# Performance work log

Measured on AMD Instinct MI355X. Metric: run time of the kernel, lower is better.

The kernel has to match this reference:

```python
import jax, jax.numpy as jnp
import numpy as np

ROI = 7
NMS_THR = 0.01
NMS_SIZE = 100


def crop_and_resize(fmap, boxes, crop):
    # fmap [H,W,C], boxes [N,4] normalized (y1,x1,y2,x2) -> [N,crop,crop,C]
    H, W, C = fmap.shape
    t = jnp.linspace(0.0, 1.0, crop)
    ys = (boxes[:, 0:1] + (boxes[:, 2:3] - boxes[:, 0:1]) * t) * (H - 1)  # [N,crop]
    xs = (boxes[:, 1:2] + (boxes[:, 3:4] - boxes[:, 1:2]) * t) * (W - 1)
    y0 = jnp.clip(jnp.floor(ys), 0, H - 1).astype(jnp.int32)
    x0 = jnp.clip(jnp.floor(xs), 0, W - 1).astype(jnp.int32)
    y1 = jnp.clip(y0 + 1, 0, H - 1)
    x1 = jnp.clip(x0 + 1, 0, W - 1)
    wy = (ys - y0)[:, :, None, None]
    wx = (xs - x0)[:, None, :, None]
    Y0, Y1 = y0[:, :, None], y1[:, :, None]
    X0, X1 = x0[:, None, :], x1[:, None, :]
    f00 = fmap[Y0, X0]; f01 = fmap[Y0, X1]
    f10 = fmap[Y1, X0]; f11 = fmap[Y1, X1]
    return (f00 * (1 - wy) * (1 - wx) + f01 * (1 - wy) * wx
            + f10 * wy * (1 - wx) + f11 * wy * wx)


def iou_matrix(b):
    # b [N,4] (x1,y1,x2,y2)
    area = jnp.maximum(b[:, 2] - b[:, 0], 0) * jnp.maximum(b[:, 3] - b[:, 1], 0)
    lt = jnp.maximum(b[:, None, :2], b[None, :, :2])
    rb = jnp.minimum(b[:, None, 2:], b[None, :, 2:])
    wh = jnp.maximum(rb - lt, 0.0)
    inter = wh[..., 0] * wh[..., 1]
    return inter / (area[:, None] + area[None, :] - inter + 1e-8)


def nms(boxes, scores, thr, max_out):
    # greedy NMS, fixed-size output (pads with lowest-ranked boxes when fewer survive)
    N = boxes.shape[0]
    order = jnp.argsort(-scores)
    M = iou_matrix(boxes[order])
    idx = jnp.arange(N)
    def body(i, keep):
        sup = (M[i] > thr) & (idx > i) & keep[i]
        return keep & ~sup
    keep = jax.lax.fori_loop(0, N, body, jnp.ones(N, dtype=bool))
    rank = jnp.where(keep, idx, N + idx)
    sel = jnp.argsort(rank)[:max_out]
    return order[sel]


def make_boxes(key, n):
    kc, ks = jax.random.split(key)
    c = jax.random.uniform(kc, (n, 2), minval=0.1, maxval=0.9)
    s = jax.random.uniform(ks, (n, 2), minval=0.02, maxval=0.15)
    lo = jnp.clip(c - s / 2, 0.0, 1.0)
    hi = jnp.clip(c + s / 2, 0.0, 1.0)
    return jnp.concatenate([lo, hi], axis=1)  # (y1,x1,y2,x2)


def setup_inputs() -> dict:
    key = jax.random.key(0)
    ks = jax.random.split(key, 12)
    N, D, Hd = 1024, ROI * ROI * 32, 2048
    img_boxes = make_boxes(ks[0], N)
    bev_boxes = make_boxes(ks[1], N)
    bev_boxes_abs = bev_boxes[:, jnp.array([1, 0, 3, 2])] * 80.0  # (x1,y1,x2,y2) in meters
    def w(k, shape, fan_in):
        return jax.random.normal(k, shape, jnp.float32) * (2.0 / fan_in) ** 0.5
    return {
        'img_feat_map': jax.random.uniform(ks[2], (1, 360, 1200, 32), jnp.float32),
        'bev_feat_map': jax.random.uniform(ks[3], (1, 700, 800, 32), jnp.float32),
        'img_boxes': img_boxes,
        'bev_boxes': bev_boxes,
        'bev_boxes_abs': bev_boxes_abs,
        'img_mask': jnp.ones((1, 1, 1, 1), jnp.float32),
        'bev_mask': jnp.ones((1, 1, 1, 1), jnp.float32),
        'W1': w(ks[4], (D, Hd), D), 'b1': jnp.zeros((Hd,), jnp.float32),
        'W2': w(ks[5], (Hd, Hd), Hd), 'b2': jnp.zeros((Hd,), jnp.float32),
        'Wc': w(ks[6], (Hd, 2), Hd), 'bc': jnp.zeros((2,), jnp.float32),
        'Wo': w(ks[7], (Hd, 10), Hd), 'bo': jnp.zeros((10,), jnp.float32),
        'Wa': w(ks[8], (Hd, 2), Hd), 'ba': jnp.zeros((2,), jnp.float32),
    }


def reference(img_feat_map, bev_feat_map, img_boxes, bev_boxes, bev_boxes_abs,
              img_mask, bev_mask, W1, b1, W2, b2, Wc, bc, Wo, bo, Wa, ba):
    # ROI align on masked feature maps
    rois_rgb = crop_and_resize((img_mask * img_feat_map)[0], img_boxes, ROI)
    rois_bev = crop_and_resize((bev_mask * bev_feat_map)[0], bev_boxes, ROI)
    # mean fusion
    fused = (rois_rgb + rois_bev) / (img_mask + bev_mask)  # [N,7,7,32]
    # predictor
    x = fused.reshape(fused.shape[0], -1)
    h = jax.nn.relu(x @ W1 + b1)
    h = jax.nn.relu(h @ W2 + b2)
    obj = h @ Wc + bc            # [N,2]
    off = h @ Wo + bo            # [N,10]
    ang = h @ Wa + ba            # [N,2]
    obj_soft = jax.nn.softmax(obj, axis=1)
    orient = jnp.arctan2(ang[:, 1], ang[:, 0])  # convert_angle_to_orientation
    # offset-adjusted BEV boxes for NMS
    pb = bev_boxes_abs + 0.1 * off[:, :4]
    boxes = jnp.stack([jnp.minimum(pb[:, 0], pb[:, 2]), jnp.minimum(pb[:, 1], pb[:, 3]),
                       jnp.maximum(pb[:, 0], pb[:, 2]), jnp.maximum(pb[:, 1], pb[:, 3])], axis=1)
    scores = jnp.max(obj[:, 1:], axis=1)
    ti = nms(jax.lax.stop_gradient(boxes), jax.lax.stop_gradient(scores), NMS_THR, NMS_SIZE)
    # [100, 2 + 4 + 1]: softmax scores, pred bev boxes, orientations
    return jnp.concatenate([obj_soft[ti], boxes[ti], orient[ti][:, None]], axis=1)
```

## Files before the change

kernel.cpp:

```cpp
#include <hip/hip_runtime.h>
#include <math.h>

#define NBOX 1024
#define ROI_N 7
#define CH 32
#define FEAT (ROI_N*ROI_N*CH)
#define K1PAD 1664
#define HD 2048
#define NMS_THR_F 0.01f
#define NMS_OUT 100
#define MTRI_WORDS 8704

typedef _Float16 f16;
typedef f16 f16x4 __attribute__((ext_vector_type(4)));
typedef f16 f16x8 __attribute__((ext_vector_type(8)));
typedef float f32x4 __attribute__((ext_vector_type(4)));

__device__ __forceinline__ void split_f16(float v, f16& h, f16& l) {
  h = (f16)v;
  l = (f16)((v - (float)h) * 4096.0f);
}

__device__ __forceinline__ void gload_lds16(const void* g, void* l) {
  __builtin_amdgcn_global_load_lds(
      (const __attribute__((address_space(1))) unsigned int*)g,
      (__attribute__((address_space(3))) unsigned int*)l, 16, 0, 0);
}

#define B_ROI 1024
#define B_C1  (64*26)
#define B_C2  (64*32)
#define B_INIT 2048
#define B_HT  112

__device__ void roi_part(int b, int tid,
    const float* __restrict__ img, const float* __restrict__ bev,
    const float* __restrict__ img_boxes, const float* __restrict__ bev_boxes,
    float mi, float mb, f16* __restrict__ xh, f16* __restrict__ xl)
{
  const float denom = mi + mb;
  if (tid >= 196) {
    const int g = tid - 196;
    if (g < 12) {
      f16x8 z = {};
      *(f16x8*)&xh[(size_t)b*K1PAD + FEAT + g*8] = z;
      *(f16x8*)&xl[(size_t)b*K1PAD + FEAT + g*8] = z;
    }
    return;
  }
  const int cell = tid >> 2, cg = (tid & 3) * 8;
  const int ti = cell / ROI_N, tj = cell - ti*ROI_N;
  const float tt_i = (ti == 6) ? 1.0f : ti * (1.0f/6.0f);
  const float tt_j = (tj == 6) ? 1.0f : tj * (1.0f/6.0f);

  float vi[8], vb[8];
  {
    const int H = 360, W = 1200;
    const float iy0 = img_boxes[b*4+0], ix0 = img_boxes[b*4+1];
    const float iy1 = img_boxes[b*4+2], ix1 = img_boxes[b*4+3];
    const float ys = (iy0 + (iy1 - iy0) * tt_i) * (float)(H-1);
    const float xs = (ix0 + (ix1 - ix0) * tt_j) * (float)(W-1);
    int y0 = (int)floorf(ys); y0 = y0 < 0 ? 0 : (y0 > H-1 ? H-1 : y0);
    int x0 = (int)floorf(xs); x0 = x0 < 0 ? 0 : (x0 > W-1 ? W-1 : x0);
    const int y1 = (y0+1 > H-1) ? H-1 : y0+1;
    const int x1 = (x0+1 > W-1) ? W-1 : x0+1;
    const float wy = ys - (float)y0, wx = xs - (float)x0;
    const float w00 = (1.0f-wy)*(1.0f-wx), w01 = (1.0f-wy)*wx;
    const float w10 = wy*(1.0f-wx),        w11 = wy*wx;
    const float* p00 = &img[(y0*W + x0)*CH + cg];
    const float* p01 = &img[(y0*W + x1)*CH + cg];
    const float* p10 = &img[(y1*W + x0)*CH + cg];
    const float* p11 = &img[(y1*W + x1)*CH + cg];
#pragma unroll
    for (int q = 0; q < 2; ++q) {
      const float4 f00 = *(const float4*)(p00 + q*4);
      const float4 f01 = *(const float4*)(p01 + q*4);
      const float4 f10 = *(const float4*)(p10 + q*4);
      const float4 f11 = *(const float4*)(p11 + q*4);
      vi[q*4+0] = f00.x*w00 + f01.x*w01 + f10.x*w10 + f11.x*w11;
      vi[q*4+1] = f00.y*w00 + f01.y*w01 + f10.y*w10 + f11.y*w11;
      vi[q*4+2] = f00.z*w00 + f01.z*w01 + f10.z*w10 + f11.z*w11;
      vi[q*4+3] = f00.w*w00 + f01.w*w01 + f10.w*w10 + f11.w*w11;
    }
  }
  {
    const int H = 700, W = 800;
    const float by0 = bev_boxes[b*4+0], bx0 = bev_boxes[b*4+1];
    const float by1 = bev_boxes[b*4+2], bx1 = bev_boxes[b*4+3];
    const float ys = (by0 + (by1 - by0) * tt_i) * (float)(H-1);
    const float xs = (bx0 + (bx1 - bx0) * tt_j) * (float)(W-1);
    int y0 = (int)floorf(ys); y0 = y0 < 0 ? 0 : (y0 > H-1 ? H-1 : y0);
    int x0 = (int)floorf(xs); x0 = x0 < 0 ? 0 : (x0 > W-1 ? W-1 : x0);
    const int y1 = (y0+1 > H-1) ? H-1 : y0+1;
    const int x1 = (x0+1 > W-1) ? W-1 : x0+1;
    const float wy = ys - (float)y0, wx = xs - (float)x0;
    const float w00 = (1.0f-wy)*(1.0f-wx), w01 = (1.0f-wy)*wx;
    const float w10 = wy*(1.0f-wx),        w11 = wy*wx;
    const float* p00 = &bev[(y0*W + x0)*CH + cg];
    const float* p01 = &bev[(y0*W + x1)*CH + cg];
    const float* p10 = &bev[(y1*W + x0)*CH + cg];
    const float* p11 = &bev[(y1*W + x1)*CH + cg];
#pragma unroll
    for (int q = 0; q < 2; ++q) {
      const float4 f00 = *(const float4*)(p00 + q*4);
      const float4 f01 = *(const float4*)(p01 + q*4);
      const float4 f10 = *(const float4*)(p10 + q*4);
      const float4 f11 = *(const float4*)(p11 + q*4);
      vb[q*4+0] = f00.x*w00 + f01.x*w01 + f10.x*w10 + f11.x*w11;
      vb[q*4+1] = f00.y*w00 + f01.y*w01 + f10.y*w10 + f11.y*w11;
      vb[q*4+2] = f00.z*w00 + f01.z*w01 + f10.z*w10 + f11.z*w11;
      vb[q*4+3] = f00.w*w00 + f01.w*w01 + f10.w*w10 + f11.w*w11;
    }
  }
  f16x8 h8, l8;
#pragma unroll
  for (int q = 0; q < 8; ++q) {
    f16 h, l;
    split_f16((mi*vi[q] + mb*vb[q]) / denom, h, l);
    h8[q] = h; l8[q] = l;
  }
  const size_t o = (size_t)b*K1PAD + cell*32 + cg;
  *(f16x8*)&xh[o] = h8;
  *(f16x8*)&xl[o] = l8;
}

__global__ __launch_bounds__(256) void prep_kernel(
    const float* __restrict__ img, const float* __restrict__ bev,
    const float* __restrict__ img_boxes, const float* __restrict__ bev_boxes,
    const float* __restrict__ img_mask, const float* __restrict__ bev_mask,
    f16* __restrict__ xh, f16* __restrict__ xl,
    const float* __restrict__ W1, f16* __restrict__ Wt1h, f16* __restrict__ Wt1l,
    const float* __restrict__ W2, f16* __restrict__ Wt2h, f16* __restrict__ Wt2l,
    const float* __restrict__ b1, const float* __restrict__ b2,
    float4* __restrict__ h1f, float4* __restrict__ h2f,
    const float* __restrict__ Wc, const float* __restrict__ Wo,
    const float* __restrict__ Wa, float* __restrict__ Wcat)
{
  __shared__ float t[64][33];
  const int g = blockIdx.x;
  const int tid = threadIdx.x;

  if (g < B_ROI) {
    roi_part(g, tid, img, bev, img_boxes, bev_boxes, img_mask[0], bev_mask[0], xh, xl);
    return;
  }
  if (g >= B_ROI + B_C1 + B_C2 + B_INIT) {
    const int idx = (g - (B_ROI + B_C1 + B_C2 + B_INIT))*256 + tid;
    const int j = idx >> 11, k = idx & (HD-1);
    float v;
    if (j < 2)       v = Wc[k*2 + j];
    else if (j < 12) v = Wo[k*10 + (j-2)];
    else             v = Wa[k*2 + (j-12)];
    Wcat[idx] = v;
    return;
  }
  const float* W; f16 *Wh, *Wl; int K, Kpad, cb;
  if (g < B_ROI + B_C1) { cb = g - B_ROI;        W = W1; Wh = Wt1h; Wl = Wt1l; K = FEAT; Kpad = K1PAD; }
  else if (g < B_ROI + B_C1 + B_C2) { cb = g - B_ROI - B_C1; W = W2; Wh = Wt2h; Wl = Wt2l; K = HD; Kpad = HD; }
  else {
    const int ib = g - B_ROI - B_C1 - B_C2;
    const int idx = ib*256 + tid;
    const int c4 = idx & (HD/4 - 1);
    h1f[idx] = *(const float4*)&b1[c4*4];
    h2f[idx] = *(const float4*)&b2[c4*4];
    return;
  }
  const int nt = cb & 63, kt = cb >> 6;
  const int n0 = nt * 32, k0 = kt * 64;
#pragma unroll
  for (int p = 0; p < 8; ++p) {
    const int idx = tid + p*256;
    const int kk = idx >> 5, nn = idx & 31;
    const int k = k0 + kk;
    t[kk][nn] = (k < K) ? W[(size_t)k*HD + n0 + nn] : 0.0f;
  }
  __syncthreads();
  const int nn = tid >> 3;
  const int kg = (tid & 7) * 8;
  f16x8 h8, l8;
#pragma unroll
  for (int q = 0; q < 8; ++q) {
    f16 h, l;
    split_f16(t[kg + q][nn], h, l);
    h8[q] = h; l8[q] = l;
  }
  *(f16x8*)&Wh[(size_t)(n0+nn)*Kpad + k0 + kg] = h8;
  *(f16x8*)&Wl[(size_t)(n0+nn)*Kpad + k0 + kg] = l8;
}

__global__ __launch_bounds__(256) void split_relu_kernel(
    const float* __restrict__ in, f16* __restrict__ oh, f16* __restrict__ ol)
{
  const int idx = blockIdx.x*256 + threadIdx.x;
  const float4 v = *(const float4*)&in[idx*4];
  f16x4 h4, l4;
  { f16 h,l; split_f16(fmaxf(v.x,0.0f),h,l); h4[0]=h; l4[0]=l; }
  { f16 h,l; split_f16(fmaxf(v.y,0.0f),h,l); h4[1]=h; l4[1]=l; }
  { f16 h,l; split_f16(fmaxf(v.z,0.0f),h,l); h4[2]=h; l4[2]=l; }
  { f16 h,l; split_f16(fmaxf(v.w,0.0f),h,l); h4[3]=h; l4[3]=l; }
  *(f16x4*)&oh[idx*4] = h4;
  *(f16x4*)&ol[idx*4] = l4;
}

#define STAGE(BUF, KK)                                                        \
  do {                                                                        \
    _Pragma("unroll")                                                         \
    for (int q_ = 0; q_ < 8; ++q_) {                                          \
      const int r_ = q_*16 + lr;                                              \
      const int sg_ = lg ^ ((r_ >> 1) & 3);                                   \
      gload_lds16(&sarr[(size_t)(rbase + r_)*K + (KK) + sg_*8],               \
                  lbase + (BUF)*16384 + q_*512);                              \
    }                                                                         \
  } while (0)

__global__ __launch_bounds__(256, 2) void gemm_sk(
    const f16* __restrict__ Ah_g, const f16* __restrict__ Al_g,
    const f16* __restrict__ Bh_g, const f16* __restrict__ Bl_g,
    float* __restrict__ Cout, int M, int N, int K, int kchunk)
{
  __shared__ __align__(16) f16 lds[2][4][128*32];
  const int tid = threadIdx.x;

  const int g = blockIdx.x;
  const int xcd = g & 7, c = g >> 3;
  const int nb = xcd*2 + (c & 1);
  const int mb = (c >> 1) & 7;
  const int zb = c >> 4;
  const int m0 = mb * 128, n0 = nb * 128;
  const int kb = zb * kchunk, ke = kb + kchunk;

  const int wid = tid >> 6, lane = tid & 63;
  const int wr = wid >> 1, wc = wid & 1;
  const int frow = lane & 15, fkg = lane >> 4;
  const int swz = (fkg ^ ((frow >> 1) & 3)) * 8;

  const f16* sarr; int rbase;
  if (wid == 0)      { sarr = Ah_g; rbase = m0; }
  else if (wid == 1) { sarr = Al_g; rbase = m0; }
  else if (wid == 2) { sarr = Bh_g; rbase = n0; }
  else               { sarr = Bl_g; rbase = n0; }
  f16* lbase = &lds[0][wid][0];
  const int lr = lane >> 2, lg = lane & 3;

  f32x4 acc1[4][4], acc2[4][4];
#pragma unroll
  for (int i = 0; i < 4; ++i)
#pragma unroll
    for (int j = 0; j < 4; ++j)
#pragma unroll
      for (int r = 0; r < 4; ++r) { acc1[i][j][r] = 0.0f; acc2[i][j][r] = 0.0f; }

  STAGE(0, kb);
  __syncthreads();
  int cur = 0;
  for (int kk = kb; kk < ke; kk += 32) {
    if (kk + 32 < ke) STAGE(cur ^ 1, kk + 32);

    const f16* bc_ = &lds[cur][0][0];
    f16x8 bh[4], bl[4];
#pragma unroll
    for (int j = 0; j < 4; ++j) {
      const int rr = wc*64 + j*16 + frow;
      bh[j] = *(const f16x8*)(bc_ + 8192  + rr*32 + swz);
      bl[j] = *(const f16x8*)(bc_ + 12288 + rr*32 + swz);
    }
#pragma unroll
    for (int i = 0; i < 4; ++i) {
      const int rr = wr*64 + i*16 + frow;
      const f16x8 ah = *(const f16x8*)(bc_ +        rr*32 + swz);
      const f16x8 al = *(const f16x8*)(bc_ + 4096 + rr*32 + swz);
#pragma unroll
      for (int j = 0; j < 4; ++j) {
        acc1[i][j] = __builtin_amdgcn_mfma_f32_16x16x32_f16(ah, bh[j], acc1[i][j], 0, 0, 0);
        acc2[i][j] = __builtin_amdgcn_mfma_f32_16x16x32_f16(ah, bl[j], acc2[i][j], 0, 0, 0);
        acc2[i][j] = __builtin_amdgcn_mfma_f32_16x16x32_f16(al, bh[j], acc2[i][j], 0, 0, 0);
      }
    }
    __syncthreads();
    cur ^= 1;
  }

  const float s = 1.0f / 4096.0f;
#pragma unroll
  for (int i = 0; i < 4; ++i)
#pragma unroll
    for (int j = 0; j < 4; ++j) {
      const int col = n0 + wc*64 + j*16 + frow;
#pragma unroll
      for (int r = 0; r < 4; ++r) {
        const int row = m0 + wr*64 + i*16 + fkg*4 + r;
        atomicAdd(&Cout[(size_t)row*N + col], acc1[i][j][r] + acc2[i][j][r] * s);
      }
    }
}

__global__ __launch_bounds__(256) void heads_kernel(
    const float* __restrict__ h2f, const float* __restrict__ Wcat,
    const float* __restrict__ bc, const float* __restrict__ bo,
    const float* __restrict__ ba, const float* __restrict__ bev_abs,
    float* __restrict__ obj_soft, float* __restrict__ boxes,
    float* __restrict__ orient, float* __restrict__ scores)
{
  const int r = blockIdx.x;
  const int tid = threadIdx.x;
  const int k0 = tid * 8;
  float4 hv0 = *(const float4*)&h2f[(size_t)r*HD + k0];
  float4 hv1 = *(const float4*)&h2f[(size_t)r*HD + k0 + 4];
  hv0.x = fmaxf(hv0.x, 0.0f); hv0.y = fmaxf(hv0.y, 0.0f);
  hv0.z = fmaxf(hv0.z, 0.0f); hv0.w = fmaxf(hv0.w, 0.0f);
  hv1.x = fmaxf(hv1.x, 0.0f); hv1.y = fmaxf(hv1.y, 0.0f);
  hv1.z = fmaxf(hv1.z, 0.0f); hv1.w = fmaxf(hv1.w, 0.0f);

  float acc[14];
#pragma unroll
  for (int j = 0; j < 14; ++j) {
    const float4 w0 = *(const float4*)&Wcat[j*HD + k0];
    const float4 w1 = *(const float4*)&Wcat[j*HD + k0 + 4];
    acc[j] = hv0.x*w0.x + hv0.y*w0.y + hv0.z*w0.z + hv0.w*w0.w
           + hv1.x*w1.x + hv1.y*w1.y + hv1.z*w1.z + hv1.w*w1.w;
  }
  __shared__ float red[14][256];
#pragma unroll
  for (int j = 0; j < 14; ++j) red[j][tid] = acc[j];
  __syncthreads();
  for (int s = 128; s > 0; s >>= 1) {
    if (tid < s) {
#pragma unroll
      for (int j = 0; j < 14; ++j) red[j][tid] += red[j][tid + s];
    }
    __syncthreads();
  }
  if (tid == 0) {
    const float obj0 = red[0][0] + bc[0];
    const float obj1 = red[1][0] + bc[1];
    const float off0 = red[2][0] + bo[0];
    const float off1 = red[3][0] + bo[1];
    const float off2 = red[4][0] + bo[2];
    const float off3 = red[5][0] + bo[3];
    const float a0 = red[12][0] + ba[0];
    const float a1 = red[13][0] + ba[1];

    const float m  = fmaxf(obj0, obj1);
    const float e0 = expf(obj0 - m), e1 = expf(obj1 - m);
    const float se = e0 + e1;
    obj_soft[r*2+0] = e0 / se;
    obj_soft[r*2+1] = e1 / se;
    orient[r] = atan2f(a1, a0);

    const float pb0 = bev_abs[r*4+0] + 0.1f*off0;
    const float pb1 = bev_abs[r*4+1] + 0.1f*off1;
    const float pb2 = bev_abs[r*4+2] + 0.1f*off2;
    const float pb3 = bev_abs[r*4+3] + 0.1f*off3;
    boxes[r*4+0] = fminf(pb0, pb2);
    boxes[r*4+1] = fminf(pb1, pb3);
    boxes[r*4+2] = fmaxf(pb0, pb2);
    boxes[r*4+3] = fmaxf(pb1, pb3);
    scores[r] = obj1;
  }
}

__global__ __launch_bounds__(128) void sort_kernel(
    const float* __restrict__ scores, const float* __restrict__ boxes,
    int* __restrict__ order, float4* __restrict__ sboxes, float* __restrict__ sarea)
{
  __shared__ float ss[NBOX];
  const int tid = threadIdx.x;
  for (int t = tid; t < NBOX; t += 128) ss[t] = scores[t];
  __syncthreads();
  const int i = blockIdx.x * 128 + tid;
  const float my = ss[i];
  int pos = 0;
  for (int j = 0; j < NBOX; ++j) {
    const float sj = ss[j];
    pos += (sj > my) || (sj == my && j < i);
  }
  const float b0 = boxes[i*4+0], b1 = boxes[i*4+1];
  const float b2 = boxes[i*4+2], b3 = boxes[i*4+3];
  order[pos]  = i;
  sboxes[pos] = make_float4(b0, b1, b2, b3);
  sarea[pos]  = fmaxf(b2 - b0, 0.0f) * fmaxf(b3 - b1, 0.0f);
}

__device__ __forceinline__ int tri_base(int i) {
  const int b = i >> 6;
  return 64*(16*b - (b*(b-1))/2) + (i & 63)*(16 - b);
}

__global__ __launch_bounds__(256) void maskbuild_kernel(
    const float4* __restrict__ sboxes, const float* __restrict__ sarea,
    unsigned long long* __restrict__ Mtri)
{
  __shared__ float4 sb[NBOX];
  __shared__ float  sa[NBOX];
  const int tid = threadIdx.x;
  for (int t = tid; t < NBOX; t += 256) { sb[t] = sboxes[t]; sa[t] = sarea[t]; }
  __syncthreads();
  const int wv = tid >> 6, lane = tid & 63;
  for (int r = 0; r < 4; ++r) {
    const int i = blockIdx.x * 16 + wv * 4 + r;
    const float4 bi = sb[i];
    const float  ai = sa[i];
    const int b = i >> 6;
    const int base = tri_base(i);
    for (int w = b; w < 16; ++w) {
      const int j = w * 64 + lane;
      const float4 bj = sb[j];
      const float lt0 = fmaxf(bi.x, bj.x), lt1 = fmaxf(bi.y, bj.y);
      const float rb0 = fminf(bi.z, bj.z), rb1 = fminf(bi.w, bj.w);
      const float wq = fmaxf(rb0 - lt0, 0.0f), hq = fmaxf(rb1 - lt1, 0.0f);
      const float inter = wq * hq;
      const float iou = inter / (ai + sa[j] - inter + 1e-8f);
      const unsigned long long bits = __ballot((j > i) && (iou > NMS_THR_F));
      if (lane == 0) Mtri[base + (w - b)] = bits;
    }
  }
}

__global__ __launch_bounds__(1024) void scan_out_kernel(
    const unsigned long long* __restrict__ Mtri_g, const int* __restrict__ order,
    const float4* __restrict__ sboxes, const float* __restrict__ obj_soft,
    const float* __restrict__ orient, float* __restrict__ out)
{
  __shared__ unsigned long long M[MTRI_WORDS];
  __shared__ unsigned long long keepw[16];
  const int tid = threadIdx.x;
  for (int t = tid; t < MTRI_WORDS; t += 1024) M[t] = Mtri_g[t];
  __syncthreads();

  if (tid < 64) {
    const int lane = tid;
    unsigned long long kw = (lane < 16) ? ~0ull : 0ull;
    for (int w = 0; w < 16; ++w) {
      unsigned long long rem = __shfl(kw, w);
      while (rem) {
        const int bpos = __builtin_ctzll(rem);
        const int i = w * 64 + bpos;
        const int base = tri_base(i);
        unsigned long long m = 0;
        if (lane >= w && lane < 16) m = M[base + (lane - w)];
        kw &= ~m;
        const unsigned long long updated = __shfl(kw, w);
        rem = (bpos == 63) ? 0ull : (updated & (~0ull << (bpos + 1)));
      }
    }
    if (lane < 16) keepw[lane] = kw;
  }
  __syncthreads();

  const int w = tid >> 6, bpos = tid & 63;
  int pre = 0, total = 0;
#pragma unroll
  for (int q = 0; q < 16; ++q) {
    const int pc = __popcll(keepw[q]);
    total += pc;
    if (q < w) pre += pc;
  }
  pre += __popcll(keepw[w] & ((bpos == 0) ? 0ull : (~0ull >> (64 - bpos))));
  const int keep_self = (int)((keepw[w] >> bpos) & 1ull);
  const int rank = keep_self ? pre : (total + tid - pre);

  if (rank < NMS_OUT) {
    const int ob = order[tid];
    const float4 bx = sboxes[tid];
    out[rank*7+0] = obj_soft[ob*2+0];
    out[rank*7+1] = obj_soft[ob*2+1];
    out[rank*7+2] = bx.x;
    out[rank*7+3] = bx.y;
    out[rank*7+4] = bx.z;
    out[rank*7+5] = bx.w;
    out[rank*7+6] = orient[ob];
  }
}

extern "C" void kernel_launch(void* const* d_in, const int* in_sizes, int n_in,
                              void* d_out, int out_size, void* d_ws, size_t ws_size,
                              hipStream_t stream) {
  (void)in_sizes; (void)n_in; (void)out_size; (void)ws_size;
  const float* img       = (const float*)d_in[0];
  const float* bev       = (const float*)d_in[1];
  const float* img_boxes = (const float*)d_in[2];
  const float* bev_boxes = (const float*)d_in[3];
  const float* bev_abs   = (const float*)d_in[4];
  const float* img_mask  = (const float*)d_in[5];
  const float* bev_mask  = (const float*)d_in[6];
  const float* W1 = (const float*)d_in[7];
  const float* b1 = (const float*)d_in[8];
  const float* W2 = (const float*)d_in[9];
  const float* b2 = (const float*)d_in[10];
  const float* Wc = (const float*)d_in[11];
  const float* bc = (const float*)d_in[12];
  const float* Wo = (const float*)d_in[13];
  const float* bo = (const float*)d_in[14];
  const float* Wa = (const float*)d_in[15];
  const float* ba = (const float*)d_in[16];
  float* out = (float*)d_out;

  char* ws = (char*)d_ws;
  f16* xh    = (f16*)ws;                                  ws += (size_t)NBOX*K1PAD*2;
  f16* xl    = (f16*)ws;                                  ws += (size_t)NBOX*K1PAD*2;
  float* h1f = (float*)ws;                                ws += (size_t)NBOX*HD*4;
  f16* h1h   = (f16*)ws;                                  ws += (size_t)NBOX*HD*2;
  f16* h1l   = (f16*)ws;                                  ws += (size_t)NBOX*HD*2;
  float* h2f = (float*)ws;                                ws += (size_t)NBOX*HD*4;
  f16* Wt1h  = (f16*)ws;                                  ws += (size_t)HD*K1PAD*2;
  f16* Wt1l  = (f16*)ws;                                  ws += (size_t)HD*K1PAD*2;
  f16* Wt2h  = (f16*)ws;                                  ws += (size_t)HD*HD*2;
  f16* Wt2l  = (f16*)ws;                                  ws += (size_t)HD*HD*2;
  float* Wcat = (float*)ws;                               ws += 14*HD*4;
  float* obj_soft = (float*)ws;                           ws += NBOX*2*4;
  float* boxesf   = (float*)ws;                           ws += NBOX*4*4;
  float* orient   = (float*)ws;                           ws += NBOX*4;
  float* scores   = (float*)ws;                           ws += NBOX*4;
  int*   order    = (int*)ws;                             ws += NBOX*4;
  float4* sboxes  = (float4*)ws;                          ws += NBOX*16;
  float* sarea    = (float*)ws;                           ws += NBOX*4;
  unsigned long long* Mtri = (unsigned long long*)ws;

  prep_kernel<<<B_ROI + B_C1 + B_C2 + B_INIT + B_HT, 256, 0, stream>>>(
      img, bev, img_boxes, bev_boxes, img_mask, bev_mask, xh, xl,
      W1, Wt1h, Wt1l, W2, Wt2h, Wt2l, b1, b2, (float4*)h1f, (float4*)h2f,
      Wc, Wo, Wa, Wcat);
  gemm_sk<<<512, 256, 0, stream>>>(xh, xl, Wt1h, Wt1l, h1f, NBOX, HD, K1PAD, K1PAD/4);
  split_relu_kernel<<<NBOX*HD/4/256, 256, 0, stream>>>(h1f, h1h, h1l);
  gemm_sk<<<512, 256, 0, stream>>>(h1h, h1l, Wt2h, Wt2l, h2f, NBOX, HD, HD, HD/4);
  heads_kernel<<<NBOX, 256, 0, stream>>>(h2f, Wcat, bc, bo, ba, bev_abs,
                                         obj_soft, boxesf, orient, scores);
  sort_kernel<<<8, 128, 0, stream>>>(scores, boxesf, order, sboxes, sarea);
  maskbuild_kernel<<<64, 256, 0, stream>>>(sboxes, sarea, Mtri);
  scan_out_kernel<<<1, 1024, 0, stream>>>(Mtri, order, sboxes, obj_soft, orient, out);
}
```

Measured before the change: 345.3 us.

## Use BK=64 single-buffer GEMM tiles and skip empty rows in NMS scan

The split-f16 GEMM now stages 64-wide K slices into a single LDS buffer with an XOR swizzle, replacing the 32-wide double-buffered pipeline. K1 padding grows to 1792 so each split-K chunk divides evenly into 64. Separately, maskbuild records which rows suppress anything in a rowAny bitmask, and the serial NMS scan visits only those rows. It also updates the in-word remainder from the row's own mask word, avoiding a shuffle per step. The costs are less load/compute overlap in the GEMM and extra zero-padding work for the first layer.

```diff
diff --git a/kernel.cpp b/kernel.cpp
--- a/kernel.cpp
+++ b/kernel.cpp
@@ -5,7 +5,7 @@
 #define ROI_N 7
 #define CH 32
 #define FEAT (ROI_N*ROI_N*CH)
-#define K1PAD 1664
+#define K1PAD 1792
 #define HD 2048
 #define NMS_THR_F 0.01f
 #define NMS_OUT 100
@@ -28,7 +28,7 @@
 }
 
 #define B_ROI 1024
-#define B_C1  (64*26)
+#define B_C1  (64*28)
 #define B_C2  (64*32)
 #define B_INIT 2048
 #define B_HT  112
@@ -41,7 +41,7 @@
   const float denom = mi + mb;
   if (tid >= 196) {
     const int g = tid - 196;
-    if (g < 12) {
+    if (g < 28) {
       f16x8 z = {};
       *(f16x8*)&xh[(size_t)b*K1PAD + FEAT + g*8] = z;
       *(f16x8*)&xl[(size_t)b*K1PAD + FEAT + g*8] = z;
@@ -134,7 +134,8 @@
     const float* __restrict__ b1, const float* __restrict__ b2,
     float4* __restrict__ h1f, float4* __restrict__ h2f,
     const float* __restrict__ Wc, const float* __restrict__ Wo,
-    const float* __restrict__ Wa, float* __restrict__ Wcat)
+    const float* __restrict__ Wa, float* __restrict__ Wcat,
+    unsigned long long* __restrict__ rowAny)
 {
   __shared__ float t[64][33];
   const int g = blockIdx.x;
@@ -163,6 +164,7 @@
     const int c4 = idx & (HD/4 - 1);
     h1f[idx] = *(const float4*)&b1[c4*4];
     h2f[idx] = *(const float4*)&b2[c4*4];
+    if (idx < 16) rowAny[idx] = 0ull;
     return;
   }
   const int nt = cb & 63, kt = cb >> 6;
@@ -202,23 +204,12 @@
   *(f16x4*)&ol[idx*4] = l4;
 }
 
-#define STAGE(BUF, KK)                                                        \
-  do {                                                                        \
-    _Pragma("unroll")                                                         \
-    for (int q_ = 0; q_ < 8; ++q_) {                                          \
-      const int r_ = q_*16 + lr;                                              \
-      const int sg_ = lg ^ ((r_ >> 1) & 3);                                   \
-      gload_lds16(&sarr[(size_t)(rbase + r_)*K + (KK) + sg_*8],               \
-                  lbase + (BUF)*16384 + q_*512);                              \
-    }                                                                         \
-  } while (0)
-
 __global__ __launch_bounds__(256, 2) void gemm_sk(
     const f16* __restrict__ Ah_g, const f16* __restrict__ Al_g,
     const f16* __restrict__ Bh_g, const f16* __restrict__ Bl_g,
     float* __restrict__ Cout, int M, int N, int K, int kchunk)
 {
-  __shared__ __align__(16) f16 lds[2][4][128*32];
+  __shared__ __align__(16) f16 lds4[4][128*64];
   const int tid = threadIdx.x;
 
   const int g = blockIdx.x;
@@ -232,15 +223,16 @@
   const int wid = tid >> 6, lane = tid & 63;
   const int wr = wid >> 1, wc = wid & 1;
   const int frow = lane & 15, fkg = lane >> 4;
-  const int swz = (fkg ^ ((frow >> 1) & 3)) * 8;
 
   const f16* sarr; int rbase;
   if (wid == 0)      { sarr = Ah_g; rbase = m0; }
   else if (wid == 1) { sarr = Al_g; rbase = m0; }
   else if (wid == 2) { sarr = Bh_g; rbase = n0; }
   else               { sarr = Bl_g; rbase = n0; }
-  f16* lbase = &lds[0][wid][0];
-  const int lr = lane >> 2, lg = lane & 3;
+  f16* lbase = &lds4[wid][0];
+  const int rowL = lane >> 3;
+  const int colOff = ((lane & 7) ^ rowL) * 8;
+  const f16* sl = sarr + (size_t)(rbase + rowL)*K + colOff;
 
   f32x4 acc1[4][4], acc2[4][4];
 #pragma unroll
@@ -250,34 +242,38 @@
 #pragma unroll
       for (int r = 0; r < 4; ++r) { acc1[i][j][r] = 0.0f; acc2[i][j][r] = 0.0f; }
 
-  STAGE(0, kb);
-  __syncthreads();
-  int cur = 0;
-  for (int kk = kb; kk < ke; kk += 32) {
-    if (kk + 32 < ke) STAGE(cur ^ 1, kk + 32);
-
-    const f16* bc_ = &lds[cur][0][0];
-    f16x8 bh[4], bl[4];
-#pragma unroll
-    for (int j = 0; j < 4; ++j) {
-      const int rr = wc*64 + j*16 + frow;
-      bh[j] = *(const f16x8*)(bc_ + 8192  + rr*32 + swz);
-      bl[j] = *(const f16x8*)(bc_ + 12288 + rr*32 + swz);
-    }
-#pragma unroll
-    for (int i = 0; i < 4; ++i) {
-      const int rr = wr*64 + i*16 + frow;
-      const f16x8 ah = *(const f16x8*)(bc_ +        rr*32 + swz);
-      const f16x8 al = *(const f16x8*)(bc_ + 4096 + rr*32 + swz);
+  for (int kk = kb; kk < ke; kk += 64) {
+    __syncthreads();
+#pragma unroll
+    for (int q = 0; q < 16; ++q)
+      gload_lds16(sl + (size_t)(q*8)*K + kk, lbase + q*512);
+    __syncthreads();
+
+#pragma unroll
+    for (int kc = 0; kc < 2; ++kc) {
+      const int qs = kc*4 + fkg;
+      f16x8 bh[4], bl[4];
 #pragma unroll
       for (int j = 0; j < 4; ++j) {
-        acc1[i][j] = __builtin_amdgcn_mfma_f32_16x16x32_f16(ah, bh[j], acc1[i][j], 0, 0, 0);
-        acc2[i][j] = __builtin_amdgcn_mfma_f32_16x16x32_f16(ah, bl[j], acc2[i][j], 0, 0, 0);
-        acc2[i][j] = __builtin_amdgcn_mfma_f32_16x16x32_f16(al, bh[j], acc2[i][j], 0, 0, 0);
+        const int rr = wc*64 + j*16 + frow;
+        const int so = rr*64 + ((qs ^ (rr & 7)) * 8);
+        bh[j] = *(const f16x8*)&lds4[2][so];
+        bl[j] = *(const f16x8*)&lds4[3][so];
       }
-    }
-    __syncthreads();
-    cur ^= 1;
+#pragma unroll
+      for (int i = 0; i < 4; ++i) {
+        const int rr = wr*64 + i*16 + frow;
+        const int so = rr*64 + ((qs ^ (rr & 7)) * 8);
+        const f16x8 ah = *(const f16x8*)&lds4[0][so];
+        const f16x8 al = *(const f16x8*)&lds4[1][so];
+#pragma unroll
+        for (int j = 0; j < 4; ++j) {
+          acc1[i][j] = __builtin_amdgcn_mfma_f32_16x16x32_f16(ah, bh[j], acc1[i][j], 0, 0, 0);
+          acc2[i][j] = __builtin_amdgcn_mfma_f32_16x16x32_f16(ah, bl[j], acc2[i][j], 0, 0, 0);
+          acc2[i][j] = __builtin_amdgcn_mfma_f32_16x16x32_f16(al, bh[j], acc2[i][j], 0, 0, 0);
+        }
+      }
+    }
   }
 
   const float s = 1.0f / 4096.0f;
@@ -388,7 +384,7 @@
 
 __global__ __launch_bounds__(256) void maskbuild_kernel(
     const float4* __restrict__ sboxes, const float* __restrict__ sarea,
-    unsigned long long* __restrict__ Mtri)
+    unsigned long long* __restrict__ Mtri, unsigned long long* __restrict__ rowAny)
 {
   __shared__ float4 sb[NBOX];
   __shared__ float  sa[NBOX];
@@ -402,6 +398,7 @@
     const float  ai = sa[i];
     const int b = i >> 6;
     const int base = tri_base(i);
+    unsigned long long any = 0;
     for (int w = b; w < 16; ++w) {
       const int j = w * 64 + lane;
       const float4 bj = sb[j];
@@ -411,27 +408,33 @@
       const float inter = wq * hq;
       const float iou = inter / (ai + sa[j] - inter + 1e-8f);
       const unsigned long long bits = __ballot((j > i) && (iou > NMS_THR_F));
+      any |= bits;
       if (lane == 0) Mtri[base + (w - b)] = bits;
     }
+    if (lane == 0 && any)
+      atomicOr(&rowAny[i >> 6], 1ull << (i & 63));
   }
 }
 
 __global__ __launch_bounds__(1024) void scan_out_kernel(
-    const unsigned long long* __restrict__ Mtri_g, const int* __restrict__ order,
-    const float4* __restrict__ sboxes, const float* __restrict__ obj_soft,
-    const float* __restrict__ orient, float* __restrict__ out)
+    const unsigned long long* __restrict__ Mtri_g, const unsigned long long* __restrict__ rowAny_g,
+    const int* __restrict__ order, const float4* __restrict__ sboxes,
+    const float* __restrict__ obj_soft, const float* __restrict__ orient,
+    float* __restrict__ out)
 {
   __shared__ unsigned long long M[MTRI_WORDS];
+  __shared__ unsigned long long rA[16];
   __shared__ unsigned long long keepw[16];
   const int tid = threadIdx.x;
   for (int t = tid; t < MTRI_WORDS; t += 1024) M[t] = Mtri_g[t];
+  if (tid < 16) rA[tid] = rowAny_g[tid];
   __syncthreads();
 
   if (tid < 64) {
     const int lane = tid;
     unsigned long long kw = (lane < 16) ? ~0ull : 0ull;
     for (int w = 0; w < 16; ++w) {
-      unsigned long long rem = __shfl(kw, w);
+      unsigned long long rem = __shfl(kw, w) & rA[w];
       while (rem) {
         const int bpos = __builtin_ctzll(rem);
         const int i = w * 64 + bpos;
@@ -439,8 +442,8 @@
         unsigned long long m = 0;
         if (lane >= w && lane < 16) m = M[base + (lane - w)];
         kw &= ~m;
-        const unsigned long long updated = __shfl(kw, w);
-        rem = (bpos == 63) ? 0ull : (updated & (~0ull << (bpos + 1)));
+        const unsigned long long m0 = M[base];
+        rem = rem & ~m0 & ((bpos == 63) ? 0ull : (~0ull << (bpos + 1)));
       }
     }
     if (lane < 16) keepw[lane] = kw;
@@ -514,18 +517,19 @@
   int*   order    = (int*)ws;                             ws += NBOX*4;
   float4* sboxes  = (float4*)ws;                          ws += NBOX*16;
   float* sarea    = (float*)ws;                           ws += NBOX*4;
-  unsigned long long* Mtri = (unsigned long long*)ws;
+  unsigned long long* Mtri = (unsigned long long*)ws;     ws += MTRI_WORDS*8;
+  unsigned long long* rowAny = (unsigned long long*)ws;   ws += 16*8;
 
   prep_kernel<<<B_ROI + B_C1 + B_C2 + B_INIT + B_HT, 256, 0, stream>>>(
       img, bev, img_boxes, bev_boxes, img_mask, bev_mask, xh, xl,
       W1, Wt1h, Wt1l, W2, Wt2h, Wt2l, b1, b2, (float4*)h1f, (float4*)h2f,
-      Wc, Wo, Wa, Wcat);
+      Wc, Wo, Wa, Wcat, rowAny);
   gemm_sk<<<512, 256, 0, stream>>>(xh, xl, Wt1h, Wt1l, h1f, NBOX, HD, K1PAD, K1PAD/4);
   split_relu_kernel<<<NBOX*HD/4/256, 256, 0, stream>>>(h1f, h1h, h1l);
   gemm_sk<<<512, 256, 0, stream>>>(h1h, h1l, Wt2h, Wt2l, h2f, NBOX, HD, HD, HD/4);
   heads_kernel<<<NBOX, 256, 0, stream>>>(h2f, Wcat, bc, bo, ba, bev_abs,
                                          obj_soft, boxesf, orient, scores);
   sort_kernel<<<8, 128, 0, stream>>>(scores, boxesf, order, sboxes, sarea);
-  maskbuild_kernel<<<64, 256, 0, stream>>>(sboxes, sarea, Mtri);
-  scan_out_kernel<<<1, 1024, 0, stream>>>(Mtri, order, sboxes, obj_soft, orient, out);
-}
+  maskbuild_kernel<<<64, 256, 0, stream>>>(sboxes, sarea, Mtri, rowAny);
+  scan_out_kernel<<<1, 1024, 0, stream>>>(Mtri, rowAny, order, sboxes, obj_soft, orient, out);
+}
```

Result: no change. 345.5 us (+0.0%).
